# Kernel tuning notes

Hardware: AMD Instinct MI355X
Metric: run time of the kernel (lower is better)

The kernel has to match this reference:

```python
import jax, jax.numpy as jnp
import numpy as np

EPS = 1e-5


def setup_inputs() -> dict:
    key = jax.random.key(0)
    ks = jax.random.split(key, 6)
    B, C, H, W = 32, 256, 32, 32
    T, O, K, KS = 256, 256, 4, 3
    return {
        "x": jax.random.normal(ks[0], (B, C, H, W), dtype=jnp.float32),
        "z": jax.random.normal(ks[1], (B, T), dtype=jnp.float32),
        "w1": jax.random.normal(ks[2], (T, T + C), dtype=jnp.float32) * 0.05,
        "bn_gamma": jnp.ones((T,), jnp.float32),
        "bn_beta": jnp.zeros((T,), jnp.float32),
        "bn_mean": jnp.zeros((T,), jnp.float32),
        "bn_var": jnp.ones((T,), jnp.float32),
        "w2": jax.random.normal(ks[3], (K, T), dtype=jnp.float32) * 0.05,
        "weight": jax.random.normal(ks[4], (K, O, C, KS, KS), dtype=jnp.float32) * 0.05,
        "static_weight": jax.random.normal(ks[5], (O, C, KS, KS), dtype=jnp.float32) * 0.05,
    }


def _kernel_attention(x, z, w1, bn_gamma, bn_beta, bn_mean, bn_var, w2):
    # x: [B,C,H,W], z: [B,T] -> att: [B,K]
    avg = jnp.mean(x, axis=(2, 3))                 # adaptive avg pool to 1x1 -> [B,C]
    a = jnp.concatenate([z, avg], axis=1)          # [B, T+C]
    h = a @ w1.T                                   # 1x1 conv on 1x1 spatial == matmul
    h = (h - bn_mean) / jnp.sqrt(bn_var + EPS) * bn_gamma + bn_beta  # BN (eval)
    h = jax.nn.relu(h)
    att = h @ w2.T                                 # [B,K]
    return jax.nn.sigmoid(att)                     # temperature = 1.0


def reference(x, z, w1, bn_gamma, bn_beta, bn_mean, bn_var, w2, weight, static_weight):
    B = x.shape[0]
    att = _kernel_attention(x, z, w1, bn_gamma, bn_beta, bn_mean, bn_var, w2)  # [B,K]
    # per-sample mixed weights: [B,O,C,k,k]
    agg_w = jnp.einsum('bk,koihw->boihw', att, weight * 0.1) + static_weight[None]

    def conv_one(xi, wi):
        # xi: [C,H,W], wi: [O,C,k,k]
        out = jax.lax.conv_general_dilated(
            xi[None], wi, window_strides=(1, 1), padding=[(1, 1), (1, 1)],
            dimension_numbers=('NCHW', 'OIHW', 'NCHW'))
        return out[0]

    return jax.vmap(conv_one)(x, agg_w)            # [B,O,H,W]
```

## Files before the change

### kernel.cpp

```cpp
#include <hip/hip_runtime.h>
#include <hip/hip_bf16.h>

typedef __attribute__((ext_vector_type(4))) float f32x4;
typedef __attribute__((ext_vector_type(8))) short bf16x8;
typedef __attribute__((ext_vector_type(8))) unsigned short ushort8;

#define EPSBN 1e-5f

__device__ __forceinline__ unsigned short f2bf(float f) {
  unsigned int u = __builtin_bit_cast(unsigned int, f);
  u += 0x7fffu + ((u >> 16) & 1u);
  return (unsigned short)(u >> 16);
}

__device__ __forceinline__ void gload_lds16(const unsigned short* g, unsigned short* l) {
  __builtin_amdgcn_global_load_lds(
      (const __attribute__((address_space(1))) void*)g,
      (__attribute__((address_space(3))) void*)l, 16, 0, 0);
}

__global__ __launch_bounds__(256) void prep_kernel(const float* __restrict__ x,
                                                   float* __restrict__ avg,
                                                   unsigned short* __restrict__ xpad) {
  int blk = blockIdx.x;
  int b = blk >> 5, cg = blk & 31;
  int t = threadIdx.x;
  int c = t >> 5, l32 = t & 31;
  __shared__ unsigned short lds_t[1024 * 9];
  __shared__ float avg_lds[8];
  const float4* xb4 = reinterpret_cast<const float4*>(x) + ((size_t)(b * 256 + cg * 8 + c)) * 256;
  float s = 0.f;
#pragma unroll
  for (int i = 0; i < 8; ++i) {
    float4 v = xb4[l32 + 32 * i];
    s += v.x + v.y + v.z + v.w;
    int p = 4 * (l32 + 32 * i);
    lds_t[(p + 0) * 9 + c] = f2bf(v.x);
    lds_t[(p + 1) * 9 + c] = f2bf(v.y);
    lds_t[(p + 2) * 9 + c] = f2bf(v.z);
    lds_t[(p + 3) * 9 + c] = f2bf(v.w);
  }
#pragma unroll
  for (int off = 16; off >= 1; off >>= 1) s += __shfl_down(s, off, 32);
  if (l32 == 0) avg_lds[c] = s;
  __syncthreads();
  if (t < 8) avg[b * 256 + cg * 8 + t] = avg_lds[t] * (1.0f / 1024.0f);
  size_t obase = (size_t)blk * 1156 * 8;
  for (int sIdx = t; sIdx < 1156; sIdx += 256) {
    int h = sIdx / 34, w = sIdx % 34;
    ushort8 v;
    if (h >= 1 && h <= 32 && w >= 1 && w <= 32) {
      int p = (h - 1) * 32 + (w - 1);
#pragma unroll
      for (int cl = 0; cl < 8; ++cl) v[cl] = lds_t[p * 9 + cl];
    } else {
#pragma unroll
      for (int cl = 0; cl < 8; ++cl) v[cl] = 0;
    }
    *reinterpret_cast<ushort8*>(xpad + obase + (size_t)sIdx * 8) = v;
  }
}

__global__ __launch_bounds__(256) void att_kernel(
    const float* __restrict__ z, const float* __restrict__ avg,
    const float* __restrict__ w1, const float* __restrict__ gamma,
    const float* __restrict__ beta, const float* __restrict__ mean,
    const float* __restrict__ var, const float* __restrict__ w2,
    float* __restrict__ att) {
  int b = blockIdx.x, t = threadIdx.x;
  __shared__ __align__(16) float a[512];
  __shared__ float h[256];
  a[t] = z[b * 256 + t];
  a[t + 256] = avg[b * 256 + t];
  __syncthreads();
  const float4* wr = reinterpret_cast<const float4*>(w1 + (size_t)t * 512);
  const float4* a4 = reinterpret_cast<const float4*>(a);
  float s = 0.f;
#pragma unroll 4
  for (int j = 0; j < 128; ++j) {
    float4 wv = wr[j], av = a4[j];
    s += wv.x * av.x + wv.y * av.y + wv.z * av.z + wv.w * av.w;
  }
  s = (s - mean[t]) * rsqrtf(var[t] + EPSBN) * gamma[t] + beta[t];
  h[t] = fmaxf(s, 0.f);
  __syncthreads();
  int wv_ = t >> 6, lane = t & 63;
  const float* w2r = w2 + wv_ * 256;
  float p = h[lane] * w2r[lane] + h[lane + 64] * w2r[lane + 64] +
            h[lane + 128] * w2r[lane + 128] + h[lane + 192] * w2r[lane + 192];
#pragma unroll
  for (int off = 32; off >= 1; off >>= 1) p += __shfl_down(p, off);
  if (lane == 0) att[b * 4 + wv_] = 1.0f / (1.0f + expf(-p));
}

#define MROW 291
__global__ __launch_bounds__(256) void mix_kernel(
    const float* __restrict__ weight, const float* __restrict__ statw,
    const float* __restrict__ att, unsigned short* __restrict__ agg) {
  int cc = blockIdx.x >> 5;
  int og = blockIdx.x & 31;
  int o0 = og * 8;
  int t = threadIdx.x;
  __shared__ float ldsf[5][8][MROW];
  __shared__ float att_lds[128];
  if (t < 128) att_lds[t] = att[t];
  const float* bases[5] = {statw, weight, weight + 589824, weight + 2 * 589824,
                           weight + 3 * 589824};
#pragma unroll
  for (int i = 0; i < 12; ++i) {
    int L = i * 256 + t;
    if (L < 2880) {
      int a = L / 576;
      int r = L % 576;
      int o_l = r / 72;
      int q = r % 72;
      float4 v = *reinterpret_cast<const float4*>(bases[a] + (size_t)(o0 + o_l) * 2304 +
                                                  cc * 288 + q * 4);
      float* d = &ldsf[a][o_l][q * 4];
      d[0] = v.x; d[1] = v.y; d[2] = v.z; d[3] = v.w;
    }
  }
  __syncthreads();
  for (int slot = t; slot < 288; slot += 256) {
    int o_l = slot & 7;
    int cblk = (slot >> 3) & 3;
    int tap = slot >> 5;
    float sv[8], wk0[8], wk1[8], wk2[8], wk3[8];
#pragma unroll
    for (int cl = 0; cl < 8; ++cl) {
      int idx9 = (cblk * 8 + cl) * 9 + tap;
      sv[cl] = ldsf[0][o_l][idx9];
      wk0[cl] = ldsf[1][o_l][idx9];
      wk1[cl] = ldsf[2][o_l][idx9];
      wk2[cl] = ldsf[3][o_l][idx9];
      wk3[cl] = ldsf[4][o_l][idx9];
    }
    size_t obase = ((size_t)(tap * 8 + cc) * 4 + cblk) * 256 + (o0 + o_l);
    for (int b = 0; b < 32; ++b) {
      float a0 = 0.1f * att_lds[b * 4 + 0];
      float a1 = 0.1f * att_lds[b * 4 + 1];
      float a2 = 0.1f * att_lds[b * 4 + 2];
      float a3 = 0.1f * att_lds[b * 4 + 3];
      ushort8 outv;
#pragma unroll
      for (int cl = 0; cl < 8; ++cl) {
        float v = sv[cl] + a0 * wk0[cl] + a1 * wk1[cl] + a2 * wk2[cl] + a3 * wk3[cl];
        outv[cl] = f2bf(v);
      }
      *reinterpret_cast<ushort8*>(agg + ((size_t)b * 73728 + obase) * 8) = outv;
    }
  }
}

__global__ __launch_bounds__(256, 2) void conv_kernel(
    const unsigned short* __restrict__ xpad, const unsigned short* __restrict__ agg,
    float* __restrict__ out) {
  int wgid = (blockIdx.x & 7) * 64 + (blockIdx.x >> 3);
  int pt = wgid & 7;
  int ot = (wgid >> 3) & 1;
  int b = wgid >> 4;
  int h0 = pt * 4;

  __shared__ __align__(16) unsigned short x_lds[2][4 * 2048];
  __shared__ __align__(16) unsigned short a_lds[2][4 * 1024];

  int tid = threadIdx.x;
  int lane = tid & 63, wv = tid >> 6;
  int wave_mo = (wv & 1) * 64;
  int wave_no = (wv >> 1) * 64;
  int kb = lane >> 4, ln = lane & 15;

  f32x4 acc[4][4];
#pragma unroll
  for (int i = 0; i < 4; ++i)
#pragma unroll
    for (int j = 0; j < 4; ++j) acc[i][j] = (f32x4){0.f, 0.f, 0.f, 0.f};

  const size_t agg_b = (size_t)b * 73728 * 8;

  auto issueA = [&](int cc, int tap, int bsel) {
    const unsigned short* g =
        agg + agg_b + (((size_t)(tap * 8 + cc) * 4 + wv) * 256 + (size_t)ot * 128) * 8;
    unsigned short* l = &a_lds[bsel][wv * 1024];
    gload_lds16(g + lane * 8, l);
    gload_lds16(g + (64 + lane) * 8, l + 512);
  };
  auto issueX = [&](int cc, int bsel) {
    const unsigned short* g = xpad + ((size_t)(b * 32 + cc * 4 + wv) * 1156 + h0 * 34) * 8;
    unsigned short* l = &x_lds[bsel][wv * 2048];
#pragma unroll
    for (int i = 0; i < 4; ++i) gload_lds16(g + i * 512 + lane * 8, l + i * 512);
  };

  int abuf = 0, xbuf = 0;
  issueX(0, 0);
  issueA(0, 0, 0);
  for (int cc = 0; cc < 8; ++cc) {
#pragma unroll
    for (int tap = 0; tap < 9; ++tap) {
      __syncthreads();
      if (tap < 8) {
        issueA(cc, tap + 1, abuf ^ 1);
      } else if (cc < 7) {
        issueA(cc + 1, 0, abuf ^ 1);
        issueX(cc + 1, xbuf ^ 1);
      }
      int dh = tap / 3, dw = tap % 3;
      bf16x8 af[4], bfr[4];
      const unsigned short* ab = &a_lds[abuf][kb * 1024];
#pragma unroll
      for (int ai = 0; ai < 4; ++ai)
        af[ai] = *reinterpret_cast<const bf16x8*>(ab + (wave_mo + ai * 16 + ln) * 8);
      const unsigned short* xb = &x_lds[xbuf][kb * 2048];
#pragma unroll
      for (int bj = 0; bj < 4; ++bj) {
        int p = wave_no + bj * 16 + ln;
        int rr = (p >> 5) + dh;
        int wc = (p & 31) + dw;
        bfr[bj] = *reinterpret_cast<const bf16x8*>(xb + (rr * 34 + wc) * 8);
      }
#pragma unroll
      for (int ai = 0; ai < 4; ++ai)
#pragma unroll
        for (int bj = 0; bj < 4; ++bj)
          acc[ai][bj] =
              __builtin_amdgcn_mfma_f32_16x16x32_bf16(af[ai], bfr[bj], acc[ai][bj], 0, 0, 0);
      abuf ^= 1;
      if (tap == 8) xbuf ^= 1;
    }
  }
  size_t ob = ((size_t)b * 256 + ot * 128 + wave_mo) * 1024 + (size_t)pt * 128 + wave_no;
#pragma unroll
  for (int ai = 0; ai < 4; ++ai)
#pragma unroll
    for (int bj = 0; bj < 4; ++bj) {
#pragma unroll
      for (int v = 0; v < 4; ++v) {
        int oo = ai * 16 + (lane >> 4) * 4 + v;
        out[ob + (size_t)oo * 1024 + bj * 16 + ln] = acc[ai][bj][v];
      }
    }
}

extern "C" void kernel_launch(void* const* d_in, const int* in_sizes, int n_in,
                              void* d_out, int out_size, void* d_ws, size_t ws_size,
                              hipStream_t stream) {
  const float* x = (const float*)d_in[0];
  const float* z = (const float*)d_in[1];
  const float* w1 = (const float*)d_in[2];
  const float* gamma = (const float*)d_in[3];
  const float* beta = (const float*)d_in[4];
  const float* mean = (const float*)d_in[5];
  const float* var = (const float*)d_in[6];
  const float* w2 = (const float*)d_in[7];
  const float* weight = (const float*)d_in[8];
  const float* statw = (const float*)d_in[9];
  float* out = (float*)d_out;

  float* att = (float*)d_ws;
  float* avg = (float*)((char*)d_ws + 1024);
  unsigned short* xpad = (unsigned short*)((char*)d_ws + 65536);
  unsigned short* agg = (unsigned short*)((char*)d_ws + 19009536);

  prep_kernel<<<1024, 256, 0, stream>>>(x, avg, xpad);
  att_kernel<<<32, 256, 0, stream>>>(z, avg, w1, gamma, beta, mean, var, w2, att);
  mix_kernel<<<256, 256, 0, stream>>>(weight, statw, att, agg);
  conv_kernel<<<512, 256, 0, stream>>>(xpad, agg, out);
}
```

Measured before the change: 92.51 us.

## Deepen conv A-tile pipeline to four LDS slots with explicit vmcnt waits

The conv kernel's weight tiles move from a double buffer to a four-slot ring with three loads in flight. The full __syncthreads per tap is replaced by explicit s_waitcnt vmcnt counts plus a raw barrier. The MFMA block is also wrapped in s_setprio. The aim is to hide global-to-LDS load latency behind compute, at the cost of more LDS and hand-tuned wait counts that must exactly match the issue order.

```diff
diff --git a/kernel.cpp b/kernel.cpp
--- a/kernel.cpp
+++ b/kernel.cpp
@@ -18,6 +18,13 @@
       (const __attribute__((address_space(1))) void*)g,
       (__attribute__((address_space(3))) void*)l, 16, 0, 0);
 }
+
+#define WAITB(N)                                          \
+  do {                                                    \
+    asm volatile("s_waitcnt vmcnt(" #N ")" ::: "memory"); \
+    __builtin_amdgcn_s_barrier();                         \
+    __builtin_amdgcn_sched_barrier(0);                    \
+  } while (0)
 
 __global__ __launch_bounds__(256) void prep_kernel(const float* __restrict__ x,
                                                    float* __restrict__ avg,
@@ -161,8 +168,8 @@
   int b = wgid >> 4;
   int h0 = pt * 4;
 
-  __shared__ __align__(16) unsigned short x_lds[2][4 * 2048];
-  __shared__ __align__(16) unsigned short a_lds[2][4 * 1024];
+  __shared__ __align__(16) unsigned short a_lds[4][4096];
+  __shared__ __align__(16) unsigned short x_lds[2][8192];
 
   int tid = threadIdx.x;
   int lane = tid & 63, wv = tid >> 6;
@@ -176,12 +183,12 @@
 #pragma unroll
     for (int j = 0; j < 4; ++j) acc[i][j] = (f32x4){0.f, 0.f, 0.f, 0.f};
 
-  const size_t agg_b = (size_t)b * 73728 * 8;
-
-  auto issueA = [&](int cc, int tap, int bsel) {
+  const size_t agg_b = (size_t)b * 589824;
+
+  auto issueA = [&](int cc, int tap, int slot) {
     const unsigned short* g =
         agg + agg_b + (((size_t)(tap * 8 + cc) * 4 + wv) * 256 + (size_t)ot * 128) * 8;
-    unsigned short* l = &a_lds[bsel][wv * 1024];
+    unsigned short* l = &a_lds[slot][wv * 1024];
     gload_lds16(g + lane * 8, l);
     gload_lds16(g + (64 + lane) * 8, l + 512);
   };
@@ -191,44 +198,71 @@
 #pragma unroll
     for (int i = 0; i < 4; ++i) gload_lds16(g + i * 512 + lane * 8, l + i * 512);
   };
-
-  int abuf = 0, xbuf = 0;
+  auto compute = [&](int cc, int tap) {
+    int slot = (cc + tap) & 3;
+    int dh = tap / 3, dw = tap % 3;
+    bf16x8 af[4], bfr[4];
+    const unsigned short* ab = &a_lds[slot][kb * 1024];
+#pragma unroll
+    for (int ai = 0; ai < 4; ++ai)
+      af[ai] = *reinterpret_cast<const bf16x8*>(ab + (wave_mo + ai * 16 + ln) * 8);
+    const unsigned short* xb = &x_lds[cc & 1][kb * 2048];
+#pragma unroll
+    for (int bj = 0; bj < 4; ++bj) {
+      int p = wave_no + bj * 16 + ln;
+      int rr = (p >> 5) + dh;
+      int wc = (p & 31) + dw;
+      bfr[bj] = *reinterpret_cast<const bf16x8*>(xb + (rr * 34 + wc) * 8);
+    }
+    __builtin_amdgcn_s_setprio(1);
+#pragma unroll
+    for (int ai = 0; ai < 4; ++ai)
+#pragma unroll
+      for (int bj = 0; bj < 4; ++bj)
+        acc[ai][bj] =
+            __builtin_amdgcn_mfma_f32_16x16x32_bf16(af[ai], bfr[bj], acc[ai][bj], 0, 0, 0);
+    __builtin_amdgcn_s_setprio(0);
+  };
+
   issueX(0, 0);
   issueA(0, 0, 0);
-  for (int cc = 0; cc < 8; ++cc) {
+  issueA(0, 1, 1);
+  issueA(0, 2, 2);
+
+  for (int cc = 0; cc < 7; ++cc) {
 #pragma unroll
     for (int tap = 0; tap < 9; ++tap) {
-      __syncthreads();
-      if (tap < 8) {
-        issueA(cc, tap + 1, abuf ^ 1);
-      } else if (cc < 7) {
-        issueA(cc + 1, 0, abuf ^ 1);
-        issueX(cc + 1, xbuf ^ 1);
+      if (tap >= 7) {
+        WAITB(8);
+      } else {
+        WAITB(4);
       }
-      int dh = tap / 3, dw = tap % 3;
-      bf16x8 af[4], bfr[4];
-      const unsigned short* ab = &a_lds[abuf][kb * 1024];
-#pragma unroll
-      for (int ai = 0; ai < 4; ++ai)
-        af[ai] = *reinterpret_cast<const bf16x8*>(ab + (wave_mo + ai * 16 + ln) * 8);
-      const unsigned short* xb = &x_lds[xbuf][kb * 2048];
-#pragma unroll
-      for (int bj = 0; bj < 4; ++bj) {
-        int p = wave_no + bj * 16 + ln;
-        int rr = (p >> 5) + dh;
-        int wc = (p & 31) + dw;
-        bfr[bj] = *reinterpret_cast<const bf16x8*>(xb + (rr * 34 + wc) * 8);
+      if (tap <= 5) {
+        issueA(cc, tap + 3, (cc + tap + 3) & 3);
+      } else if (tap == 6) {
+        issueX(cc + 1, (cc + 1) & 1);
+        issueA(cc + 1, 0, (cc + 1) & 3);
+      } else if (tap == 7) {
+        issueA(cc + 1, 1, (cc + 2) & 3);
+      } else {
+        issueA(cc + 1, 2, (cc + 3) & 3);
       }
-#pragma unroll
-      for (int ai = 0; ai < 4; ++ai)
-#pragma unroll
-        for (int bj = 0; bj < 4; ++bj)
-          acc[ai][bj] =
-              __builtin_amdgcn_mfma_f32_16x16x32_bf16(af[ai], bfr[bj], acc[ai][bj], 0, 0, 0);
-      abuf ^= 1;
-      if (tap == 8) xbuf ^= 1;
-    }
-  }
+      compute(cc, tap);
+    }
+  }
+#pragma unroll
+  for (int tap = 0; tap < 9; ++tap) {
+    if (tap == 7) {
+      WAITB(2);
+    } else if (tap == 8) {
+      WAITB(0);
+    } else {
+      WAITB(4);
+    }
+    if (tap <= 5) issueA(7, tap + 3, (7 + tap + 3) & 3);
+    compute(7, tap);
+  }
+
   size_t ob = ((size_t)b * 256 + ot * 128 + wave_mo) * 1024 + (size_t)pt * 128 + wave_no;
 #pragma unroll
   for (int ai = 0; ai < 4; ++ai)
```

Result: no change. 93.43 us (+1.0%).

## Load aggregated weights directly into registers, drop A LDS buffer and per-tap barriers

Applied to the files above, without the earlier changes.

The per-sample mixed weights now go straight from global memory into registers, with the next tap prefetched one step ahead. The A tile is no longer staged in LDS. This removes the A shared-memory buffer and the barrier on every tap, so there is one __syncthreads per channel chunk, and LDS use drops. s_setprio is also raised around the MFMA block. The risk is exposed global-load latency, because each wave fetches its own A fragments and the 64-wave neighbours of the same tile each fetch them redundantly.

```diff
diff --git a/kernel.cpp b/kernel.cpp
--- a/kernel.cpp
+++ b/kernel.cpp
@@ -161,8 +161,7 @@
   int b = wgid >> 4;
   int h0 = pt * 4;
 
-  __shared__ __align__(16) unsigned short x_lds[2][4 * 2048];
-  __shared__ __align__(16) unsigned short a_lds[2][4 * 1024];
+  __shared__ __align__(16) unsigned short x_lds[2][8192];
 
   int tid = threadIdx.x;
   int lane = tid & 63, wv = tid >> 6;
@@ -176,15 +175,9 @@
 #pragma unroll
     for (int j = 0; j < 4; ++j) acc[i][j] = (f32x4){0.f, 0.f, 0.f, 0.f};
 
-  const size_t agg_b = (size_t)b * 73728 * 8;
-
-  auto issueA = [&](int cc, int tap, int bsel) {
-    const unsigned short* g =
-        agg + agg_b + (((size_t)(tap * 8 + cc) * 4 + wv) * 256 + (size_t)ot * 128) * 8;
-    unsigned short* l = &a_lds[bsel][wv * 1024];
-    gload_lds16(g + lane * 8, l);
-    gload_lds16(g + (64 + lane) * 8, l + 512);
-  };
+  const unsigned short* aggL =
+      agg + (size_t)b * 589824 + ((size_t)kb * 256 + ot * 128 + wave_mo + ln) * 8;
+
   auto issueX = [&](int cc, int bsel) {
     const unsigned short* g = xpad + ((size_t)(b * 32 + cc * 4 + wv) * 1156 + h0 * 34) * 8;
     unsigned short* l = &x_lds[bsel][wv * 2048];
@@ -192,26 +185,29 @@
     for (int i = 0; i < 4; ++i) gload_lds16(g + i * 512 + lane * 8, l + i * 512);
   };
 
-  int abuf = 0, xbuf = 0;
   issueX(0, 0);
-  issueA(0, 0, 0);
+  __syncthreads();
+
+  bf16x8 af[4];
+#pragma unroll 1
   for (int cc = 0; cc < 8; ++cc) {
+    if (cc < 7) issueX(cc + 1, (cc + 1) & 1);
+    const unsigned short* aggC = aggL + (size_t)(0 * 8 + cc) * 8192;
+#pragma unroll
+    for (int ai = 0; ai < 4; ++ai)
+      af[ai] = *reinterpret_cast<const bf16x8*>(aggC + (size_t)ai * 128);
+    const unsigned short* xb = &x_lds[cc & 1][kb * 2048];
 #pragma unroll
     for (int tap = 0; tap < 9; ++tap) {
-      __syncthreads();
+      bf16x8 afn[4];
       if (tap < 8) {
-        issueA(cc, tap + 1, abuf ^ 1);
-      } else if (cc < 7) {
-        issueA(cc + 1, 0, abuf ^ 1);
-        issueX(cc + 1, xbuf ^ 1);
+        const unsigned short* aggN = aggL + (size_t)((tap + 1) * 8 + cc) * 8192;
+#pragma unroll
+        for (int ai = 0; ai < 4; ++ai)
+          afn[ai] = *reinterpret_cast<const bf16x8*>(aggN + (size_t)ai * 128);
       }
       int dh = tap / 3, dw = tap % 3;
-      bf16x8 af[4], bfr[4];
-      const unsigned short* ab = &a_lds[abuf][kb * 1024];
-#pragma unroll
-      for (int ai = 0; ai < 4; ++ai)
-        af[ai] = *reinterpret_cast<const bf16x8*>(ab + (wave_mo + ai * 16 + ln) * 8);
-      const unsigned short* xb = &x_lds[xbuf][kb * 2048];
+      bf16x8 bfr[4];
 #pragma unroll
       for (int bj = 0; bj < 4; ++bj) {
         int p = wave_no + bj * 16 + ln;
@@ -219,16 +215,22 @@
         int wc = (p & 31) + dw;
         bfr[bj] = *reinterpret_cast<const bf16x8*>(xb + (rr * 34 + wc) * 8);
       }
+      __builtin_amdgcn_s_setprio(1);
 #pragma unroll
       for (int ai = 0; ai < 4; ++ai)
 #pragma unroll
         for (int bj = 0; bj < 4; ++bj)
           acc[ai][bj] =
               __builtin_amdgcn_mfma_f32_16x16x32_bf16(af[ai], bfr[bj], acc[ai][bj], 0, 0, 0);
-      abuf ^= 1;
-      if (tap == 8) xbuf ^= 1;
-    }
-  }
+      __builtin_amdgcn_s_setprio(0);
+      if (tap < 8) {
+#pragma unroll
+        for (int ai = 0; ai < 4; ++ai) af[ai] = afn[ai];
+      }
+    }
+    __syncthreads();
+  }
+
   size_t ob = ((size_t)b * 256 + ot * 128 + wave_mo) * 1024 + (size_t)pt * 128 + wave_no;
 #pragma unroll
   for (int ai = 0; ai < 4; ++ai)
```

Result: faster. 83.86 us (-9.4%).
